# Kernel optimization log

Measured on AMD Instinct MI355X. Metric: run time of the kernel, lower is better.

## Reference

```python
import jax, jax.numpy as jnp
import numpy as np

OUTPUT_SIZE = 512


def _build_schedule(n, m):
    """Static pyramid-circuit schedule of Givens/RBS gates on n wires.

    Sequential gate order (matches theta ordering): for k = 1..n-1, apply
    gates on adjacent wire pairs (i, i+1) for i = k-1 down to max(k-m, 0).
    Total gates = (2n - m - 1) * m // 2. Gates are packed into a brickwork
    schedule (timestep t = 2(k-1) - i) so each layer touches disjoint pairs
    and the whole chain runs in T = n + m - 2 parallel layers.
    Padded slots point at dummy wires (n, n+1) and are masked to identity.
    """
    layers = {}
    t_idx = 0
    for k in range(1, n):
        for i in range(k - 1, max(k - m, 0) - 1, -1):
            t = 2 * (k - 1) - i
            layers.setdefault(t, []).append((i, t_idx))
            t_idx += 1
    T = max(layers) + 1
    W = max(len(v) for v in layers.values())
    wire = np.full((T, W), n, dtype=np.int32)   # pad gates hit dummy wires (n, n+1)
    tidx = np.zeros((T, W), dtype=np.int32)
    mask = np.zeros((T, W), dtype=np.float32)
    for t, gs in layers.items():
        for j, (i, ti) in enumerate(gs):
            wire[t, j] = i
            tidx[t, j] = ti
            mask[t, j] = 1.0
    return wire, tidx, mask


def apply_orthogonal(thetas, x, output_size):
    input_size = x.shape[-1]
    n, m = max(input_size, output_size), min(input_size, output_size)
    wire, tidx, mask = _build_schedule(n, m)
    if input_size < n:
        x = jnp.pad(x, ((0, 0), (0, n - input_size)))
    state = jnp.pad(x, ((0, 0), (0, 2)))          # two dummy columns for padded gate slots
    th = thetas[jnp.asarray(tidx)]                # [T, W]
    msk = jnp.asarray(mask)
    cos = jnp.where(msk > 0, jnp.cos(th), 1.0)    # padded slots -> identity rotation
    sin = jnp.where(msk > 0, jnp.sin(th), 0.0)
    wa = jnp.asarray(wire)                        # [T, W] first wire of each pair
    wb = wa + 1

    def step(st, layer):
        c, s, a_idx, b_idx = layer
        a = st[:, a_idx]                          # [B, W]
        b = st[:, b_idx]
        st = st.at[:, a_idx].set(c * a + s * b)   # RBS rotation on each pair
        st = st.at[:, b_idx].set(c * b - s * a)
        return st, None

    state, _ = jax.lax.scan(step, state, (cos, sin, wa, wb))
    return state[:, :output_size]


def setup_inputs():
    key = jax.random.key(0)
    k1, k2 = jax.random.split(key)
    B, N = 256, 512
    n_thetas = (2 * max(N, OUTPUT_SIZE) - min(N, OUTPUT_SIZE) - 1) * min(N, OUTPUT_SIZE) // 2
    x = jax.random.normal(k1, (B, N), dtype=jnp.float32)
    thetas = jax.random.uniform(k2, (n_thetas,), dtype=jnp.float32,
                                minval=-np.pi, maxval=np.pi)
    bias = jnp.zeros((OUTPUT_SIZE,), dtype=jnp.float32)
    return {"x": x, "thetas": thetas, "bias": bias}


def reference(x, thetas, bias):
    # normalize_inputs=False path; with_bias=True
    out = apply_orthogonal(thetas, x, OUTPUT_SIZE)
    return out + bias
```

## Files before the change

### kernel.cpp

```cpp
#include <hip/hip_runtime.h>
#include <hip/hip_fp16.h>
#include <stdint.h>


#define NWIN 8
#define WPAIRS 64
#define V_ELEMS (512 * 512)

#define OFF_P_BYTES (4u << 20)
#define OFF_Q_BYTES (6u << 20)

typedef _Float16 half8_t __attribute__((ext_vector_type(8)));
typedef float f32x4_t __attribute__((ext_vector_type(4)));

template <int N>
__device__ __forceinline__ void wait_vm() {
  asm volatile("s_waitcnt vmcnt(%0)" ::"i"(N) : "memory");
}
template <int CTRL>
__device__ __forceinline__ float dpp_f(float v) {
  return __int_as_float(
      __builtin_amdgcn_mov_dpp(__float_as_int(v), CTRL, 0xF, 0xF, true));
}
template <int CTRL>
__device__ __forceinline__ uint32_t dpp_u(uint32_t v) {
  return (uint32_t)__builtin_amdgcn_mov_dpp((int)v, CTRL, 0xF, 0xF, true);
}
__device__ __forceinline__ uint32_t pk2(float a, float b) {
  return __builtin_bit_cast(uint32_t, __builtin_amdgcn_cvt_pkrtz(a, b));
}
__device__ __forceinline__ float mix_s(uint32_t g, float b) {
  float d;
  asm("v_fma_mix_f32 %0, %1, %2, 0 op_sel:[1,0,0] op_sel_hi:[1,0,0]"
      : "=v"(d) : "v"(g), "v"(b));
  return d;
}
__device__ __forceinline__ float mix_ns(uint32_t g, float b) {
  float d;
  asm("v_fma_mix_f32 %0, -%1, %2, 0 op_sel:[1,0,0] op_sel_hi:[1,0,0]"
      : "=v"(d) : "v"(g), "v"(b));
  return d;
}
__device__ __forceinline__ float mix_c_acc(uint32_t g, float b, float acc) {
  float d;
  asm("v_fma_mix_f32 %0, %1, %2, %3 op_sel:[0,0,0] op_sel_hi:[1,0,0]"
      : "=v"(d) : "v"(g), "v"(b), "v"(acc));
  return d;
}
__device__ __forceinline__ void gate_mix(float& a, float& b, uint32_t g) {
  float t = mix_s(g, b);
  float u = mix_ns(g, a);
  float na = mix_c_acc(g, a, t);
  float nb = mix_c_acc(g, b, u);
  a = na; b = nb;
}
__device__ __forceinline__ void gate_mix_neg(float& a, float& b, uint32_t g) {
  float t = mix_ns(g, b);
  float u = mix_s(g, a);
  float na = mix_c_acc(g, a, t);
  float nb = mix_c_acc(g, b, u);
  a = na; b = nb;
}

__device__ __forceinline__ void pair_fwd(float& v0, float& v1, float& v2,
                                         float& v3, float& v4, float& v5,
                                         float& v6, float& v7,
                                         const uint4& E, const uint4& O) {
  gate_mix(v0, v1, E.x);
  gate_mix(v2, v3, E.y);
  gate_mix(v4, v5, E.z);
  gate_mix(v6, v7, E.w);
  uint32_t bl = dpp_u<0x111>(O.w);
  float rv0 = dpp_f<0x101>(v0);
  float lv7 = dpp_f<0x111>(v7);
  gate_mix(v1, v2, O.x);
  gate_mix(v3, v4, O.y);
  gate_mix(v5, v6, O.z);
  float t = mix_s(O.w, rv0);
  t = mix_c_acc(O.w, v7, t);
  v7 = t + v7;
  float u = mix_ns(bl, lv7);
  u = mix_c_acc(bl, v0, u);
  v0 = u + v0;
}

__device__ __forceinline__ void pair_rev(float& v0, float& v1, float& v2,
                                         float& v3, float& v4, float& v5,
                                         float& v6, float& v7,
                                         const uint4& E, const uint4& O) {
  uint32_t bl = dpp_u<0x111>(O.w);
  float rv0 = dpp_f<0x101>(v0);
  float lv7 = dpp_f<0x111>(v7);
  gate_mix_neg(v1, v2, O.x);
  gate_mix_neg(v3, v4, O.y);
  gate_mix_neg(v5, v6, O.z);
  float t = mix_ns(O.w, rv0);
  t = mix_c_acc(O.w, v7, t);
  v7 = t + v7;
  float u = mix_s(bl, lv7);
  u = mix_c_acc(bl, v0, u);
  v0 = u + v0;
  gate_mix_neg(v0, v1, E.x);
  gate_mix_neg(v2, v3, E.y);
  gate_mix_neg(v4, v5, E.z);
  gate_mix_neg(v6, v7, E.w);
}

__global__ __launch_bounds__(256) void winblock_kernel(
    const float* __restrict__ thetas, _Float16* __restrict__ V) {
  __shared__ uint4 ldsq[2560];
  const int bid = blockIdx.x;
  const int tid = threadIdx.x;
  const int w = bid >> 5;
  const int d0 = (bid & 31) << 4;
  const int p0 = w * WPAIRS;
  int bb = d0 - 60;
  int base0 = (bb <= 0) ? 0 : (bb & ~7);
  base0 = min(base0, 384);
  const int L0 = base0 >> 3;

#pragma unroll
  for (int kk = 0; kk < 10; ++kk) {
    int slot = tid + (kk << 8);
    int p = slot / 40;
    int r = slot - p * 40;
    int h = r / 20;
    int Ls = r - h * 20;
    int t = 2 * (p0 + p) + h;
    int Lg = L0 + Ls;
    uint32_t gq[4];
#pragma unroll
    for (int j = 0; j < 4; ++j) {
      int i = 8 * Lg + 2 * j + h;
      float c = 1.0f, s = 0.0f;
      if (i <= min(t, 1020 - t)) {
        int k2 = ((t + i) >> 1) + 1;
        int idx = ((k2 * (k2 - 1)) >> 1) + (k2 - 1 - i);
        __sincosf(thetas[idx], &s, &c);
      }
      if (h == 1 && j == 3) c -= 1.0f;
      gq[j] = __builtin_bit_cast(uint32_t, __floats2half2_rn(c, s));
    }
    ldsq[slot] = make_uint4(gq[0], gq[1], gq[2], gq[3]);
  }
  __syncthreads();

  const int lane = tid & 63;
  const int wv = tid >> 6;
  const int gl = lane & 15, grp = lane >> 4;
  const int d = d0 + wv * 4 + grp;
  const bool rev = (w & 1);
  int b1 = d - 60;
  int base = (b1 <= 0) ? 0 : (b1 & ~7);
  base = min(base, 384);
  const int ls = ((base >> 3) - L0) + gl;
  const int wire0 = base + 8 * gl;

  float v0 = (wire0 + 0 == d) ? 1.f : 0.f;
  float v1 = (wire0 + 1 == d) ? 1.f : 0.f;
  float v2 = (wire0 + 2 == d) ? 1.f : 0.f;
  float v3 = (wire0 + 3 == d) ? 1.f : 0.f;
  float v4 = (wire0 + 4 == d) ? 1.f : 0.f;
  float v5 = (wire0 + 5 == d) ? 1.f : 0.f;
  float v6 = (wire0 + 6 == d) ? 1.f : 0.f;
  float v7 = (wire0 + 7 == d) ? 1.f : 0.f;

  uint4 R[4][2];
  if (!rev) {
#pragma unroll
    for (int s = 0; s < 4; ++s) {
      R[s][0] = ldsq[s * 40 + ls];
      R[s][1] = ldsq[s * 40 + 20 + ls];
    }
    for (int it = 0; it < 16; ++it) {
#pragma unroll
      for (int s = 0; s < 4; ++s) {
        pair_fwd(v0, v1, v2, v3, v4, v5, v6, v7, R[s][0], R[s][1]);
        int pn = min(it * 4 + s + 4, 63);
        R[s][0] = ldsq[pn * 40 + ls];
        R[s][1] = ldsq[pn * 40 + 20 + ls];
      }
    }
  } else {
#pragma unroll
    for (int s = 0; s < 4; ++s) {
      R[s][0] = ldsq[(63 - s) * 40 + ls];
      R[s][1] = ldsq[(63 - s) * 40 + 20 + ls];
    }
    for (int it = 0; it < 16; ++it) {
#pragma unroll
      for (int s = 0; s < 4; ++s) {
        pair_rev(v0, v1, v2, v3, v4, v5, v6, v7, R[s][0], R[s][1]);
        int pn = max(59 - it * 4 - s, 0);
        R[s][0] = ldsq[pn * 40 + ls];
        R[s][1] = ldsq[pn * 40 + 20 + ls];
      }
    }
  }

  uint32_t ph0 = pk2(v0, v1);
  uint32_t ph1 = pk2(v2, v3);
  uint32_t ph2 = pk2(v4, v5);
  uint32_t ph3 = pk2(v6, v7);
  uint32_t* dst = (uint32_t*)(V + (size_t)w * V_ELEMS + (size_t)d * 512);
#pragma unroll
  for (int pass = 0; pass < 4; ++pass) {
    const int S = ((pass << 7) - base) >> 3;
    const int srcg = gl + S;
    const bool ok = (srcg >= 0) && (srcg < 16);
    const int baddr = ((grp << 4) + (ok ? srcg : 0)) << 2;
    uint32_t o0 = (uint32_t)__builtin_amdgcn_ds_bpermute(baddr, (int)ph0);
    uint32_t o1 = (uint32_t)__builtin_amdgcn_ds_bpermute(baddr, (int)ph1);
    uint32_t o2 = (uint32_t)__builtin_amdgcn_ds_bpermute(baddr, (int)ph2);
    uint32_t o3 = (uint32_t)__builtin_amdgcn_ds_bpermute(baddr, (int)ph3);
    if (!ok) { o0 = 0u; o1 = 0u; o2 = 0u; o3 = 0u; }
    *(uint4*)(dst + pass * 64 + gl * 4) = make_uint4(o0, o1, o2, o3);
  }
}

struct GemmDesc { const _Float16* A; const _Float16* B; _Float16* C; };
struct Descs4 { GemmDesc d[4]; };

__global__ __launch_bounds__(128) void gemm512_kernel(Descs4 ds) {
  const int g = blockIdx.x >> 7;
  const int t = blockIdx.x & 127;
  const int rt = t >> 3, ct = t & 7;
  const int lane = threadIdx.x & 63, wv = threadIdx.x >> 6;
  const int l16 = lane & 15, h8 = (lane >> 4) * 8;
  const GemmDesc de = ds.d[g];
  const _Float16* Ap = de.A + (size_t)(rt * 32 + wv * 16 + l16) * 512 + h8;
  const _Float16* Bp = de.B + (size_t)(ct * 64 + l16) * 512 + h8;

  half8_t aR[3]; half8_t bR[3][4];
#pragma unroll
  for (int s = 0; s < 3; ++s) {
    aR[s] = *(const half8_t*)(Ap + s * 32);
#pragma unroll
    for (int n = 0; n < 4; ++n)
      bR[s][n] = *(const half8_t*)(Bp + (size_t)n * (16 * 512) + s * 32);
  }
  f32x4_t acc[4];
#pragma unroll
  for (int n = 0; n < 4; ++n) acc[n] = (f32x4_t){0.f, 0.f, 0.f, 0.f};

#pragma unroll
  for (int ks = 0; ks < 16; ++ks) {
    const int s = ks % 3;
    if (ks <= 13) wait_vm<10>();
    else if (ks == 14) wait_vm<5>();
    else wait_vm<0>();
    half8_t a = aR[s];
    half8_t b0 = bR[s][0], b1 = bR[s][1], b2 = bR[s][2], b3 = bR[s][3];
    if (ks + 3 < 16) {
      aR[s] = *(const half8_t*)(Ap + (ks + 3) * 32);
#pragma unroll
      for (int n = 0; n < 4; ++n)
        bR[s][n] = *(const half8_t*)(Bp + (size_t)n * (16 * 512) + (ks + 3) * 32);
    }
    acc[0] = __builtin_amdgcn_mfma_f32_16x16x32_f16(a, b0, acc[0], 0, 0, 0);
    acc[1] = __builtin_amdgcn_mfma_f32_16x16x32_f16(a, b1, acc[1], 0, 0, 0);
    acc[2] = __builtin_amdgcn_mfma_f32_16x16x32_f16(a, b2, acc[2], 0, 0, 0);
    acc[3] = __builtin_amdgcn_mfma_f32_16x16x32_f16(a, b3, acc[3], 0, 0, 0);
  }
  const int r4 = rt * 32 + wv * 16 + (lane >> 4) * 4;
#pragma unroll
  for (int n = 0; n < 4; ++n) {
    uint2 pk;
    pk.x = pk2(acc[n][0], acc[n][1]);
    pk.y = pk2(acc[n][2], acc[n][3]);
    *(uint2*)(de.C + (size_t)(ct * 64 + n * 16 + l16) * 512 + r4) = pk;
  }
}

__global__ __launch_bounds__(256, 1) void applyf_kernel(
    const _Float16* __restrict__ Qt0, const _Float16* __restrict__ Qt1,
    const float* __restrict__ x, const float* __restrict__ bias,
    float* __restrict__ out) {
  __shared__ float yT[16 * 516];
  const int b = blockIdx.x;
  const int tid = threadIdx.x;
  const int lane = tid & 63, wv = tid >> 6;
  const int l16 = lane & 15, hh = lane >> 4;
  const int h8 = hh * 8;

  {
    const float* Bx = x + (size_t)(b * 16 + l16) * 512 + h8;
    const _Float16* Ap = Qt0 + (size_t)(wv * 128 + l16) * 512 + h8;
    half8_t aR[2][8]; float4 fR[2][2];
#pragma unroll
    for (int s = 0; s < 2; ++s) {
      fR[s][0] = *(const float4*)(Bx + s * 32);
      fR[s][1] = *(const float4*)(Bx + s * 32 + 4);
#pragma unroll
      for (int r = 0; r < 8; ++r)
        aR[s][r] = *(const half8_t*)(Ap + (size_t)r * (16 * 512) + s * 32);
    }
    f32x4_t acc[8];
#pragma unroll
    for (int r = 0; r < 8; ++r) acc[r] = (f32x4_t){0.f, 0.f, 0.f, 0.f};

#pragma unroll
    for (int ks = 0; ks < 16; ++ks) {
      const int s = ks & 1;
      if (ks < 14) wait_vm<10>();
      else wait_vm<0>();
      float4 f0 = fR[s][0], f1 = fR[s][1];
      half8_t aC[8];
#pragma unroll
      for (int r = 0; r < 8; ++r) aC[r] = aR[s][r];
      if (ks + 2 < 16) {
        const int ko = (ks + 2) * 32;
        fR[s][0] = *(const float4*)(Bx + ko);
        fR[s][1] = *(const float4*)(Bx + ko + 4);
#pragma unroll
        for (int r = 0; r < 8; ++r)
          aR[s][r] = *(const half8_t*)(Ap + (size_t)r * (16 * 512) + ko);
      }
      uint4 u;
      u.x = pk2(f0.x, f0.y);
      u.y = pk2(f0.z, f0.w);
      u.z = pk2(f1.x, f1.y);
      u.w = pk2(f1.z, f1.w);
      half8_t bf = __builtin_bit_cast(half8_t, u);
#pragma unroll
      for (int r = 0; r < 8; ++r)
        acc[r] = __builtin_amdgcn_mfma_f32_16x16x32_f16(aC[r], bf, acc[r], 0, 0, 0);
    }
#pragma unroll
    for (int r = 0; r < 8; ++r) {
      const int w0 = wv * 128 + r * 16 + hh * 4;
#pragma unroll
      for (int jj = 0; jj < 4; ++jj)
        yT[l16 * 516 + w0 + jj] = acc[r][jj];
    }
  }
  __syncthreads();

  {
    const _Float16* Ap = Qt1 + (size_t)(wv * 128 + l16) * 512 + h8;
    const float* By = &yT[l16 * 516 + h8];
    half8_t aR[2][8];
#pragma unroll
    for (int s = 0; s < 2; ++s)
#pragma unroll
      for (int r = 0; r < 8; ++r)
        aR[s][r] = *(const half8_t*)(Ap + (size_t)r * (16 * 512) + s * 32);
    f32x4_t acc[8];
#pragma unroll
    for (int r = 0; r < 8; ++r) acc[r] = (f32x4_t){0.f, 0.f, 0.f, 0.f};

#pragma unroll
    for (int ks = 0; ks < 16; ++ks) {
      const int s = ks & 1;
      if (ks < 14) wait_vm<8>();
      else wait_vm<0>();
      half8_t aC[8];
#pragma unroll
      for (int r = 0; r < 8; ++r) aC[r] = aR[s][r];
      if (ks + 2 < 16) {
        const int ko = (ks + 2) * 32;
#pragma unroll
        for (int r = 0; r < 8; ++r)
          aR[s][r] = *(const half8_t*)(Ap + (size_t)r * (16 * 512) + ko);
      }
      float4 f0 = *(const float4*)(By + ks * 32);
      float4 f1 = *(const float4*)(By + ks * 32 + 4);
      uint4 u;
      u.x = pk2(f0.x, f0.y);
      u.y = pk2(f0.z, f0.w);
      u.z = pk2(f1.x, f1.y);
      u.w = pk2(f1.z, f1.w);
      half8_t bf = __builtin_bit_cast(half8_t, u);
#pragma unroll
      for (int r = 0; r < 8; ++r)
        acc[r] = __builtin_amdgcn_mfma_f32_16x16x32_f16(aC[r], bf, acc[r], 0, 0, 0);
    }
#pragma unroll
    for (int r = 0; r < 8; ++r) {
      const int w0 = wv * 128 + r * 16 + hh * 4;
      const float4 bv = *(const float4*)(bias + w0);
      float4 o;
      o.x = acc[r][0] + bv.x;
      o.y = acc[r][1] + bv.y;
      o.z = acc[r][2] + bv.z;
      o.w = acc[r][3] + bv.w;
      *(float4*)(out + (size_t)(b * 16 + l16) * 512 + w0) = o;
    }
  }
}

extern "C" void kernel_launch(void* const* d_in, const int* in_sizes, int n_in,
                              void* d_out, int out_size, void* d_ws,
                              size_t ws_size, hipStream_t stream) {
  const float* x = (const float*)d_in[0];
  const float* thetas = (const float*)d_in[1];
  const float* bias = (const float*)d_in[2];
  float* out = (float*)d_out;

  char* ws = (char*)d_ws;
  _Float16* V = (_Float16*)ws;
  _Float16* P = (_Float16*)(ws + OFF_P_BYTES);
  _Float16* Q = (_Float16*)(ws + OFF_Q_BYTES);

  winblock_kernel<<<256, 256, 0, stream>>>(thetas, V);

  Descs4 l1;
  l1.d[0] = {V + 1 * (size_t)V_ELEMS, V + 0 * (size_t)V_ELEMS, P + 0 * (size_t)V_ELEMS};
  l1.d[1] = {V + 2 * (size_t)V_ELEMS, V + 3 * (size_t)V_ELEMS, P + 1 * (size_t)V_ELEMS};
  l1.d[2] = {V + 5 * (size_t)V_ELEMS, V + 4 * (size_t)V_ELEMS, P + 2 * (size_t)V_ELEMS};
  l1.d[3] = {V + 6 * (size_t)V_ELEMS, V + 7 * (size_t)V_ELEMS, P + 3 * (size_t)V_ELEMS};
  gemm512_kernel<<<512, 128, 0, stream>>>(l1);

  Descs4 l2;
  l2.d[0] = {P + 0 * (size_t)V_ELEMS, P + 1 * (size_t)V_ELEMS, Q + 0 * (size_t)V_ELEMS};
  l2.d[1] = {P + 2 * (size_t)V_ELEMS, P + 3 * (size_t)V_ELEMS, Q + 1 * (size_t)V_ELEMS};
  l2.d[2] = l2.d[0];
  l2.d[3] = l2.d[0];
  gemm512_kernel<<<256, 128, 0, stream>>>(l2);

  applyf_kernel<<<16, 256, 0, stream>>>(Q, Q + (size_t)V_ELEMS, x, bias, out);
}
```

Measured before the change: 130.0 us.

## Precompute gate cos/sin table in separate kernel and stream it from global memory

Splits the old winblock kernel into two kernels. The first computes every gate's fp16 cos/sin pair once into a global table. The second is a 64-thread-per-block window kernel that streams gate quads from global memory with explicit vmcnt waits, where the old kernel staged them through LDS. This removes the sincos work that overlapping blocks repeated and raises block count for occupancy. In exchange it adds a kernel launch, a global write and read of the table, and exposes global-load latency inside the serial gate loop.

Result: faster. 126.1 us (-3.0%).

```diff
diff --git a/kernel.cpp b/kernel.cpp
--- a/kernel.cpp
+++ b/kernel.cpp
@@ -3,15 +3,35 @@
 #include <stdint.h>
 
 
+#define PAIRS_PAD 512
+#define TOTALH2 (PAIRS_PAD * 512)
 #define NWIN 8
 #define WPAIRS 64
 #define V_ELEMS (512 * 512)
 
-#define OFF_P_BYTES (4u << 20)
-#define OFF_Q_BYTES (6u << 20)
+#define OFF_V_BYTES (1u << 20)
+#define OFF_P_BYTES (5u << 20)
+#define OFF_Q_BYTES (7u << 20)
 
 typedef _Float16 half8_t __attribute__((ext_vector_type(8)));
 typedef float f32x4_t __attribute__((ext_vector_type(4)));
+
+__global__ __launch_bounds__(256) void fused_kernel(
+    const float* __restrict__ thetas, __half2* __restrict__ Wh) {
+  int tid = blockIdx.x * 256 + threadIdx.x;
+  int p = tid >> 9, r = tid & 511;
+  int h = r >> 8, rr = r & 255, L = rr >> 2, j = rr & 3;
+  int t = 2 * p + h;
+  int i = 8 * L + 2 * j + h;
+  float c = 1.0f, s = 0.0f;
+  if (i <= min(t, 1020 - t)) {
+    int k = ((t + i) >> 1) + 1;
+    int idx = ((k * (k - 1)) >> 1) + (k - 1 - i);
+    __sincosf(thetas[idx], &s, &c);
+  }
+  if (h == 1 && j == 3) c -= 1.0f;
+  Wh[tid] = __floats2half2_rn(c, s);
+}
 
 template <int N>
 __device__ __forceinline__ void wait_vm() {
@@ -106,54 +126,17 @@
   gate_mix_neg(v6, v7, E.w);
 }
 
-__global__ __launch_bounds__(256) void winblock_kernel(
-    const float* __restrict__ thetas, _Float16* __restrict__ V) {
-  __shared__ uint4 ldsq[2560];
-  const int bid = blockIdx.x;
-  const int tid = threadIdx.x;
-  const int w = bid >> 5;
-  const int d0 = (bid & 31) << 4;
-  const int p0 = w * WPAIRS;
-  int bb = d0 - 60;
-  int base0 = (bb <= 0) ? 0 : (bb & ~7);
-  base0 = min(base0, 384);
-  const int L0 = base0 >> 3;
-
-#pragma unroll
-  for (int kk = 0; kk < 10; ++kk) {
-    int slot = tid + (kk << 8);
-    int p = slot / 40;
-    int r = slot - p * 40;
-    int h = r / 20;
-    int Ls = r - h * 20;
-    int t = 2 * (p0 + p) + h;
-    int Lg = L0 + Ls;
-    uint32_t gq[4];
-#pragma unroll
-    for (int j = 0; j < 4; ++j) {
-      int i = 8 * Lg + 2 * j + h;
-      float c = 1.0f, s = 0.0f;
-      if (i <= min(t, 1020 - t)) {
-        int k2 = ((t + i) >> 1) + 1;
-        int idx = ((k2 * (k2 - 1)) >> 1) + (k2 - 1 - i);
-        __sincosf(thetas[idx], &s, &c);
-      }
-      if (h == 1 && j == 3) c -= 1.0f;
-      gq[j] = __builtin_bit_cast(uint32_t, __floats2half2_rn(c, s));
-    }
-    ldsq[slot] = make_uint4(gq[0], gq[1], gq[2], gq[3]);
-  }
-  __syncthreads();
-
-  const int lane = tid & 63;
-  const int wv = tid >> 6;
+__global__ __launch_bounds__(64) void window_kernel(
+    const uint32_t* __restrict__ W, _Float16* __restrict__ V) {
+  const int lane = threadIdx.x;
   const int gl = lane & 15, grp = lane >> 4;
-  const int d = d0 + wv * 4 + grp;
+  const int w = blockIdx.x >> 7;
+  const int d = ((blockIdx.x & 127) << 2) + grp;
   const bool rev = (w & 1);
-  int b1 = d - 60;
-  int base = (b1 <= 0) ? 0 : (b1 & ~7);
+  int b0 = d - 60;
+  int base = (b0 <= 0) ? 0 : (b0 & ~7);
   base = min(base, 384);
-  const int ls = ((base >> 3) - L0) + gl;
+  const int idx0 = (base >> 3) + gl;
   const int wire0 = base + 8 * gl;
 
   float v0 = (wire0 + 0 == d) ? 1.f : 0.f;
@@ -165,35 +148,40 @@
   float v6 = (wire0 + 6 == d) ? 1.f : 0.f;
   float v7 = (wire0 + 7 == d) ? 1.f : 0.f;
 
+  const int p0 = w * WPAIRS;
+  const uint4* __restrict__ Wg = (const uint4*)W;
+
   uint4 R[4][2];
   if (!rev) {
 #pragma unroll
     for (int s = 0; s < 4; ++s) {
-      R[s][0] = ldsq[s * 40 + ls];
-      R[s][1] = ldsq[s * 40 + 20 + ls];
+      R[s][0] = Wg[(p0 + s) * 128 + idx0];
+      R[s][1] = Wg[(p0 + s) * 128 + 64 + idx0];
     }
     for (int it = 0; it < 16; ++it) {
 #pragma unroll
       for (int s = 0; s < 4; ++s) {
+        wait_vm<6>();
         pair_fwd(v0, v1, v2, v3, v4, v5, v6, v7, R[s][0], R[s][1]);
-        int pn = min(it * 4 + s + 4, 63);
-        R[s][0] = ldsq[pn * 40 + ls];
-        R[s][1] = ldsq[pn * 40 + 20 + ls];
+        int pn = p0 + min(it * 4 + s + 4, 63);
+        R[s][0] = Wg[pn * 128 + idx0];
+        R[s][1] = Wg[pn * 128 + 64 + idx0];
       }
     }
   } else {
 #pragma unroll
     for (int s = 0; s < 4; ++s) {
-      R[s][0] = ldsq[(63 - s) * 40 + ls];
-      R[s][1] = ldsq[(63 - s) * 40 + 20 + ls];
+      R[s][0] = Wg[(p0 + 63 - s) * 128 + idx0];
+      R[s][1] = Wg[(p0 + 63 - s) * 128 + 64 + idx0];
     }
     for (int it = 0; it < 16; ++it) {
 #pragma unroll
       for (int s = 0; s < 4; ++s) {
+        wait_vm<6>();
         pair_rev(v0, v1, v2, v3, v4, v5, v6, v7, R[s][0], R[s][1]);
-        int pn = max(59 - it * 4 - s, 0);
-        R[s][0] = ldsq[pn * 40 + ls];
-        R[s][1] = ldsq[pn * 40 + 20 + ls];
+        int pn = p0 + 63 - min(it * 4 + s + 4, 63);
+        R[s][0] = Wg[pn * 128 + idx0];
+        R[s][1] = Wg[pn * 128 + 64 + idx0];
       }
     }
   }
@@ -398,11 +386,13 @@
   float* out = (float*)d_out;
 
   char* ws = (char*)d_ws;
-  _Float16* V = (_Float16*)ws;
+  uint32_t* W = (uint32_t*)ws;
+  _Float16* V = (_Float16*)(ws + OFF_V_BYTES);
   _Float16* P = (_Float16*)(ws + OFF_P_BYTES);
   _Float16* Q = (_Float16*)(ws + OFF_Q_BYTES);
 
-  winblock_kernel<<<256, 256, 0, stream>>>(thetas, V);
+  fused_kernel<<<TOTALH2 / 256, 256, 0, stream>>>(thetas, (__half2*)W);
+  window_kernel<<<NWIN * 128, 64, 0, stream>>>(W, V);
 
   Descs4 l1;
   l1.d[0] = {V + 1 * (size_t)V_ELEMS, V + 0 * (size_t)V_ELEMS, P + 0 * (size_t)V_ELEMS};
```
